# Kernel tuning notes

Measured on AMD Instinct MI355X. Metric: run time of the kernel, lower is better.

Reference implementation:

```python
import jax, jax.numpy as jnp
import numpy as np
import math

B, S, H, D = 1, 2048, 32, 128  # batch, local_seq (one ring block), num_heads, head_dim


def setup_inputs() -> dict:
    key = jax.random.key(0)
    kq, kk, kv = jax.random.split(key, 3)
    return {
        "query": jax.random.normal(kq, (B, S, H, D), dtype=jnp.float32),
        "key": jax.random.normal(kk, (B, S, H, D), dtype=jnp.float32),
        "value": jax.random.normal(kv, (B, S, H, D), dtype=jnp.float32),
    }


def reference(query, key, value):
    # RingAttention with world_size=1: a single ring step where q_block_idx == kv_block_idx,
    # i.e. standard causal attention on the local block. The online-softmax update from the
    # initial (output=0, lse=-inf) accumulator is the identity, so it is omitted.
    b, s, h, d = query.shape
    scale = 1.0 / math.sqrt(d)
    # [b, h, q, k] scores
    scores = jnp.einsum("bqhd,bkhd->bhqk", query, key) * scale
    causal = jnp.triu(jnp.ones((s, s), dtype=bool), k=1)  # True above diagonal -> masked
    scores = jnp.where(causal[None, None, :, :], -jnp.inf, scores)
    probs = jax.nn.softmax(scores, axis=-1)
    out = jnp.einsum("bhqk,bkhd->bqhd", probs, value)
    return out
```

## Files before the change

kernel.cpp:

```cpp
#include <hip/hip_runtime.h>
#include <hip/hip_bf16.h>
#include <stdint.h>

#define SEQ   2048
#define NHEAD 32
#define HDIM  128
#define RS    (NHEAD * HDIM)
#define KVBLK 64
#define NTILES (SEQ / KVBLK)
#define TILE_BYTES 16384

typedef float  f32x16 __attribute__((ext_vector_type(16)));
typedef __bf16 bf16x8 __attribute__((ext_vector_type(8)));
typedef uint32_t u32;

__device__ __forceinline__ unsigned short f2bf(float f) {
  unsigned u = __builtin_bit_cast(unsigned, f);
  u += 0x7fffu + ((u >> 16) & 1u);
  return (unsigned short)(u >> 16);
}

__device__ __forceinline__ u32 packbf(float a, float b) {
  __bf16 x = (__bf16)a, y = (__bf16)b;
  unsigned short ux = __builtin_bit_cast(unsigned short, x);
  unsigned short uy = __builtin_bit_cast(unsigned short, y);
  return (u32)ux | ((u32)uy << 16);
}

__global__ __launch_bounds__(256) void prepass_kernel(
    const float* __restrict__ K, const float* __restrict__ V,
    char* __restrict__ wsK, char* __restrict__ wsV) {
  const int tid = threadIdx.x;
  const int t   = blockIdx.x & (NTILES - 1);
  const int h   = blockIdx.x >> 5;
  const int kv0 = t * KVBLK;
  char* kd = wsK + (size_t)(h * NTILES + t) * TILE_BYTES;
  char* vd = wsV + (size_t)(h * NTILES + t) * TILE_BYTES;

  {
    const int c  = tid & 15;
    const int kr = tid >> 4;
#pragma unroll
    for (int ki = 0; ki < 4; ++ki) {
      const int kk = kr + ki * 16;
      const float* kp = K + (size_t)(kv0 + kk) * RS + h * HDIM + c * 8;
      float4 x0 = *(const float4*)kp;
      float4 x1 = *(const float4*)(kp + 4);
      uint32_t u0 = f2bf(x0.x) | ((uint32_t)f2bf(x0.y) << 16);
      uint32_t u1 = f2bf(x0.z) | ((uint32_t)f2bf(x0.w) << 16);
      uint32_t u2 = f2bf(x1.x) | ((uint32_t)f2bf(x1.y) << 16);
      uint32_t u3 = f2bf(x1.z) | ((uint32_t)f2bf(x1.w) << 16);
      const int kt = kk >> 5, n = kk & 31, ks = c >> 1, hh = c & 1;
      const uint32_t byte = (uint32_t)((kt * 8 + ks) * 1024 + (hh * 32 + n) * 16);
      *(uint4*)(kd + byte) = make_uint4(u0, u1, u2, u3);
    }
  }
  {
    const int d0  = (tid & 31) * 4;
    const int kk0 = (tid >> 5) * 8;
    float vv[8][4];
#pragma unroll
    for (int r = 0; r < 8; ++r) {
      const float* vp = V + (size_t)(kv0 + kk0 + r) * RS + h * HDIM + d0;
      float4 x = *(const float4*)vp;
      vv[r][0] = x.x; vv[r][1] = x.y; vv[r][2] = x.z; vv[r][3] = x.w;
    }
    const int s = kk0 >> 4, hh = (kk0 >> 3) & 1;
#pragma unroll
    for (int i = 0; i < 4; ++i) {
      const int d = d0 + i;
      uint32_t p0 = f2bf(vv[0][i]) | ((uint32_t)f2bf(vv[1][i]) << 16);
      uint32_t p1 = f2bf(vv[2][i]) | ((uint32_t)f2bf(vv[3][i]) << 16);
      uint32_t p2 = f2bf(vv[4][i]) | ((uint32_t)f2bf(vv[5][i]) << 16);
      uint32_t p3 = f2bf(vv[6][i]) | ((uint32_t)f2bf(vv[7][i]) << 16);
      const int nt = d >> 5;
      const uint32_t byte = (uint32_t)((s * 4 + nt) * 1024 + (hh * 32 + (d & 31)) * 16);
      *(uint4*)(vd + byte) = make_uint4(p0, p1, p2, p3);
    }
  }
}

__global__ __launch_bounds__(64, 2) void fattn_main(
    const float* __restrict__ Q, const char* __restrict__ wsK,
    const char* __restrict__ wsV, float* __restrict__ O) {
  const int lane = threadIdx.x;
  const int n    = lane & 31;
  const int hh   = lane >> 5;

  const int bid  = blockIdx.x;
  const int k    = bid >> 3;
  const int head = (bid & 7) * 4 + (k & 3);
  const int qi   = 63 - (k >> 2);
  const int ntile = (qi >> 1) + 1;
  const int qrow  = qi * 32 + n;

  const float qscale = 0.088388347648318447f * 1.4426950408889634f;

  bf16x8 bq[8];
  {
    const float* qp = Q + (size_t)qrow * RS + head * HDIM + hh * 8;
#pragma unroll
    for (int ks = 0; ks < 8; ++ks) {
      float4 v0 = *(const float4*)(qp + ks * 16);
      float4 v1 = *(const float4*)(qp + ks * 16 + 4);
      bf16x8 a;
      a[0] = (__bf16)(v0.x * qscale); a[1] = (__bf16)(v0.y * qscale);
      a[2] = (__bf16)(v0.z * qscale); a[3] = (__bf16)(v0.w * qscale);
      a[4] = (__bf16)(v1.x * qscale); a[5] = (__bf16)(v1.y * qscale);
      a[6] = (__bf16)(v1.z * qscale); a[7] = (__bf16)(v1.w * qscale);
      bq[ks] = a;
    }
  }

  f32x16 accO[4];
#pragma unroll
  for (int i = 0; i < 4; ++i) accO[i] = (f32x16)(0.f);
  float m_run  = -1e30f;
  float l_part = 0.f;

  const char* kimg = wsK + (size_t)head * NTILES * TILE_BYTES;
  const char* vimg = wsV + (size_t)head * NTILES * TILE_BYTES;

  for (int t = 0; t < ntile; ++t) {
    const char* kb = kimg + (size_t)t * TILE_BYTES + lane * 16;
    uint4 kld[16];
#pragma unroll
    for (int i = 0; i < 16; ++i) kld[i] = *(const uint4*)(kb + i * 1024);

    f32x16 sc[2];
    __builtin_amdgcn_s_setprio(1);
#pragma unroll
    for (int kt = 0; kt < 2; ++kt) {
      f32x16 acc = (f32x16)(0.f);
#pragma unroll
      for (int ks = 0; ks < 8; ++ks) {
        bf16x8 kf = __builtin_bit_cast(bf16x8, kld[kt * 8 + ks]);
        acc = __builtin_amdgcn_mfma_f32_32x32x16_bf16(kf, bq[ks], acc, 0, 0, 0);
      }
      sc[kt] = acc;
    }
    __builtin_amdgcn_s_setprio(0);

    const char* vb = vimg + (size_t)t * TILE_BYTES + lane * 16;
    uint4 vld[16];
#pragma unroll
    for (int i = 0; i < 16; ++i) vld[i] = *(const uint4*)(vb + i * 1024);

    if (t == ntile - 1) {
      const int kv0 = t * KVBLK;
#pragma unroll
      for (int kt = 0; kt < 2; ++kt)
#pragma unroll
        for (int r = 0; r < 16; ++r) {
          const int keyg = kv0 + kt * 32 + (r & 3) + 8 * (r >> 2) + 4 * hh;
          if (keyg > qrow) sc[kt][r] = -1e30f;
        }
    }

    float mx = -1e30f;
#pragma unroll
    for (int kt = 0; kt < 2; ++kt)
#pragma unroll
      for (int r = 0; r < 16; ++r) mx = fmaxf(mx, sc[kt][r]);
    mx = fmaxf(mx, __shfl_xor(mx, 32, 64));

    if (__any(mx - m_run > 11.0f)) {
      const float mn = fmaxf(m_run, mx);
      const float al = exp2f(m_run - mn);
      m_run = mn;
      l_part *= al;
#pragma unroll
      for (int r = 0; r < 16; ++r) {
        const float ar = __shfl(al, (r & 3) + 8 * (r >> 2) + 4 * hh, 64);
#pragma unroll
        for (int nt = 0; nt < 4; ++nt) accO[nt][r] *= ar;
      }
    }

    float ls = 0.f;
#pragma unroll
    for (int kt = 0; kt < 2; ++kt)
#pragma unroll
      for (int r = 0; r < 16; ++r) {
        const float p = exp2f(sc[kt][r] - m_run);
        sc[kt][r] = p;
        ls += p;
      }
    l_part += ls;

    u32 ua[2][4], ub[2][4];
#pragma unroll
    for (int kt = 0; kt < 2; ++kt)
#pragma unroll
      for (int i = 0; i < 4; ++i) {
        ua[kt][i] = packbf(sc[kt][4 * i],     sc[kt][4 * i + 1]);
        ub[kt][i] = packbf(sc[kt][4 * i + 2], sc[kt][4 * i + 3]);
      }
    u32 ra[2][2], rb[2][2];
#pragma unroll
    for (int kt = 0; kt < 2; ++kt)
#pragma unroll
      for (int q = 0; q < 2; ++q) {
        ra[kt][q] = __shfl_xor(hh ? ua[kt][2 * q] : ua[kt][2 * q + 1], 32, 64);
        rb[kt][q] = __shfl_xor(hh ? ub[kt][2 * q] : ub[kt][2 * q + 1], 32, 64);
      }

    __builtin_amdgcn_s_setprio(1);
#pragma unroll
    for (int s = 0; s < 4; ++s) {
      const int kt = s >> 1, q = s & 1;
      u32 af32[4];
      af32[0] = hh ? ra[kt][q] : ua[kt][2 * q];
      af32[1] = hh ? rb[kt][q] : ub[kt][2 * q];
      af32[2] = hh ? ua[kt][2 * q + 1] : ra[kt][q];
      af32[3] = hh ? ub[kt][2 * q + 1] : rb[kt][q];
      bf16x8 af = __builtin_bit_cast(bf16x8, *(uint4*)af32);
#pragma unroll
      for (int nt = 0; nt < 4; ++nt) {
        bf16x8 vf = __builtin_bit_cast(bf16x8, vld[s * 4 + nt]);
        accO[nt] = __builtin_amdgcn_mfma_f32_32x32x16_bf16(af, vf, accO[nt], 0, 0, 0);
      }
    }
    __builtin_amdgcn_s_setprio(0);
  }

  const float lf  = l_part + __shfl_xor(l_part, 32, 64);
  const float inv = 1.0f / lf;
  float* ob = O + (size_t)(qi * 32) * RS + head * HDIM;
#pragma unroll
  for (int r = 0; r < 16; ++r) {
    const int m = (r & 3) + 8 * (r >> 2) + 4 * hh;
    const float im = __shfl(inv, m, 64);
#pragma unroll
    for (int nt = 0; nt < 4; ++nt)
      ob[(size_t)m * RS + nt * 32 + n] = accO[nt][r] * im;
  }
}

extern "C" void kernel_launch(void* const* d_in, const int* in_sizes, int n_in,
                              void* d_out, int out_size, void* d_ws, size_t ws_size,
                              hipStream_t stream) {
  const float* q = (const float*)d_in[0];
  const float* k = (const float*)d_in[1];
  const float* v = (const float*)d_in[2];
  float* o = (float*)d_out;
  char* wsK = (char*)d_ws;
  char* wsV = wsK + (size_t)NHEAD * NTILES * TILE_BYTES;
  hipLaunchKernelGGL(prepass_kernel, dim3(NHEAD * NTILES), dim3(256), 0, stream,
                     k, v, wsK, wsV);
  hipLaunchKernelGGL(fattn_main, dim3(2048), dim3(64), 0, stream, q, wsK, wsV, o);
}
```

Measured before the change: 89.10 us.

## Prefetch next K tile and split V loads to overlap with MFMA

Loads the first K tile before the loop, then inside each iteration prefetches the next K tile after the QK^T MFMAs. V is split into two halves: the first is issued before the score MFMAs and the second after, so global load latency overlaps with compute instead of stalling each tile. The row max is also rewritten as a tree reduction to shorten the dependency chain. This raises register pressure (K prefetch plus V halves live at once), which at 2 waves per SIMD could cause spills or lower occupancy.

```diff
diff --git a/kernel.cpp b/kernel.cpp
--- a/kernel.cpp
+++ b/kernel.cpp
@@ -118,14 +118,18 @@
   float m_run  = -1e30f;
   float l_part = 0.f;
 
-  const char* kimg = wsK + (size_t)head * NTILES * TILE_BYTES;
-  const char* vimg = wsV + (size_t)head * NTILES * TILE_BYTES;
+  const char* kimg = wsK + (size_t)head * NTILES * TILE_BYTES + lane * 16;
+  const char* vimg = wsV + (size_t)head * NTILES * TILE_BYTES + lane * 16;
+
+  uint4 kld[16];
+#pragma unroll
+  for (int i = 0; i < 16; ++i) kld[i] = *(const uint4*)(kimg + i * 1024);
 
   for (int t = 0; t < ntile; ++t) {
-    const char* kb = kimg + (size_t)t * TILE_BYTES + lane * 16;
-    uint4 kld[16];
-#pragma unroll
-    for (int i = 0; i < 16; ++i) kld[i] = *(const uint4*)(kb + i * 1024);
+    const char* vb = vimg + (size_t)t * TILE_BYTES;
+    uint4 vldA[8];
+#pragma unroll
+    for (int i = 0; i < 8; ++i) vldA[i] = *(const uint4*)(vb + i * 1024);
 
     f32x16 sc[2];
     __builtin_amdgcn_s_setprio(1);
@@ -141,10 +145,15 @@
     }
     __builtin_amdgcn_s_setprio(0);
 
-    const char* vb = vimg + (size_t)t * TILE_BYTES + lane * 16;
-    uint4 vld[16];
-#pragma unroll
-    for (int i = 0; i < 16; ++i) vld[i] = *(const uint4*)(vb + i * 1024);
+    if (t + 1 < ntile) {
+      const char* kb = kimg + (size_t)(t + 1) * TILE_BYTES;
+#pragma unroll
+      for (int i = 0; i < 16; ++i) kld[i] = *(const uint4*)(kb + i * 1024);
+    }
+
+    uint4 vldB[8];
+#pragma unroll
+    for (int i = 0; i < 8; ++i) vldB[i] = *(const uint4*)(vb + (i + 8) * 1024);
 
     if (t == ntile - 1) {
       const int kv0 = t * KVBLK;
@@ -157,11 +166,14 @@
         }
     }
 
-    float mx = -1e30f;
-#pragma unroll
-    for (int kt = 0; kt < 2; ++kt)
-#pragma unroll
-      for (int r = 0; r < 16; ++r) mx = fmaxf(mx, sc[kt][r]);
+    float tm[16];
+#pragma unroll
+    for (int r = 0; r < 16; ++r) tm[r] = fmaxf(sc[0][r], sc[1][r]);
+#pragma unroll
+    for (int r = 0; r < 8; ++r) tm[r] = fmaxf(tm[r], tm[r + 8]);
+#pragma unroll
+    for (int r = 0; r < 4; ++r) tm[r] = fmaxf(tm[r], tm[r + 4]);
+    float mx = fmaxf(fmaxf(tm[0], tm[1]), fmaxf(tm[2], tm[3]));
     mx = fmaxf(mx, __shfl_xor(mx, 32, 64));
 
     if (__any(mx - m_run > 11.0f)) {
@@ -217,7 +229,8 @@
       bf16x8 af = __builtin_bit_cast(bf16x8, *(uint4*)af32);
 #pragma unroll
       for (int nt = 0; nt < 4; ++nt) {
-        bf16x8 vf = __builtin_bit_cast(bf16x8, vld[s * 4 + nt]);
+        const uint4 vchunk = (s < 2) ? vldA[s * 4 + nt] : vldB[(s - 2) * 4 + nt];
+        bf16x8 vf = __builtin_bit_cast(bf16x8, vchunk);
         accO[nt] = __builtin_amdgcn_mfma_f32_32x32x16_bf16(af, vf, accO[nt], 0, 0, 0);
       }
     }
```

New measurement: 160.4 us. +80.0%, slower.

## Split each causal query block's KV loop in two and merge partials

Applied to the files above, without the earlier changes.

Each query block's KV tiles are now processed by two workgroups, one taking even tiles and one taking odd tiles. Each writes an unnormalized fp32 partial output plus its row max and sum to workspace. A new combine kernel rescales the two partials, merges them and normalizes. The aim is more parallelism and shorter per-workgroup loops on long causal rows. The cost is about 64MB of extra partial writes and reads, one more launch, and a dependence on the workspace being large enough, with the old single-pass kernel kept as a fallback.

```diff
diff --git a/kernel.cpp b/kernel.cpp
--- a/kernel.cpp
+++ b/kernel.cpp
@@ -9,6 +9,7 @@
 #define KVBLK 64
 #define NTILES (SEQ / KVBLK)
 #define TILE_BYTES 16384
+#define IMG_BYTES ((size_t)NHEAD * NTILES * TILE_BYTES)
 
 typedef float  f32x16 __attribute__((ext_vector_type(16)));
 typedef __bf16 bf16x8 __attribute__((ext_vector_type(8)));
@@ -50,8 +51,8 @@
       uint32_t u1 = f2bf(x0.z) | ((uint32_t)f2bf(x0.w) << 16);
       uint32_t u2 = f2bf(x1.x) | ((uint32_t)f2bf(x1.y) << 16);
       uint32_t u3 = f2bf(x1.z) | ((uint32_t)f2bf(x1.w) << 16);
-      const int kt = kk >> 5, n = kk & 31, ks = c >> 1, hh = c & 1;
-      const uint32_t byte = (uint32_t)((kt * 8 + ks) * 1024 + (hh * 32 + n) * 16);
+      const int kt = kk >> 5, nn = kk & 31, ks = c >> 1, hh = c & 1;
+      const uint32_t byte = (uint32_t)((kt * 8 + ks) * 1024 + (hh * 32 + nn) * 16);
       *(uint4*)(kd + byte) = make_uint4(u0, u1, u2, u3);
     }
   }
@@ -80,149 +81,207 @@
   }
 }
 
-__global__ __launch_bounds__(64, 2) void fattn_main(
+#define FLASH_BODY(T0, STEP)                                                     \
+  for (int t = (T0); t < ntile; t += (STEP)) {                                   \
+    const char* kb = kimg + (size_t)t * TILE_BYTES;                              \
+    uint4 kld[16];                                                               \
+    _Pragma("unroll")                                                            \
+    for (int i = 0; i < 16; ++i) kld[i] = *(const uint4*)(kb + i * 1024);        \
+    f32x16 sc[2];                                                                \
+    __builtin_amdgcn_s_setprio(1);                                               \
+    _Pragma("unroll")                                                            \
+    for (int kt = 0; kt < 2; ++kt) {                                             \
+      f32x16 acc = (f32x16)(0.f);                                                \
+      _Pragma("unroll")                                                          \
+      for (int ks = 0; ks < 8; ++ks) {                                           \
+        bf16x8 kf = __builtin_bit_cast(bf16x8, kld[kt * 8 + ks]);                \
+        acc = __builtin_amdgcn_mfma_f32_32x32x16_bf16(kf, bq[ks], acc, 0, 0, 0); \
+      }                                                                          \
+      sc[kt] = acc;                                                              \
+    }                                                                            \
+    __builtin_amdgcn_s_setprio(0);                                               \
+    const char* vb = vimg + (size_t)t * TILE_BYTES;                              \
+    uint4 vld[16];                                                               \
+    _Pragma("unroll")                                                            \
+    for (int i = 0; i < 16; ++i) vld[i] = *(const uint4*)(vb + i * 1024);        \
+    if (t == ntile - 1) {                                                        \
+      const int kv0 = t * KVBLK;                                                 \
+      _Pragma("unroll")                                                          \
+      for (int kt = 0; kt < 2; ++kt)                                             \
+        _Pragma("unroll")                                                        \
+        for (int r = 0; r < 16; ++r) {                                           \
+          const int keyg = kv0 + kt * 32 + (r & 3) + 8 * (r >> 2) + 4 * hh;      \
+          if (keyg > qrow) sc[kt][r] = -1e30f;                                   \
+        }                                                                        \
+    }                                                                            \
+    float tm[16];                                                                \
+    _Pragma("unroll")                                                            \
+    for (int r = 0; r < 16; ++r) tm[r] = fmaxf(sc[0][r], sc[1][r]);              \
+    _Pragma("unroll")                                                            \
+    for (int r = 0; r < 8; ++r) tm[r] = fmaxf(tm[r], tm[r + 8]);                 \
+    _Pragma("unroll")                                                            \
+    for (int r = 0; r < 4; ++r) tm[r] = fmaxf(tm[r], tm[r + 4]);                 \
+    float mx = fmaxf(fmaxf(tm[0], tm[1]), fmaxf(tm[2], tm[3]));                  \
+    mx = fmaxf(mx, __shfl_xor(mx, 32, 64));                                      \
+    if (__any(mx - m_run > 11.0f)) {                                             \
+      const float mn = fmaxf(m_run, mx);                                         \
+      const float al = exp2f(m_run - mn);                                        \
+      m_run = mn;                                                                \
+      l_part *= al;                                                              \
+      _Pragma("unroll")                                                          \
+      for (int r = 0; r < 16; ++r) {                                             \
+        const float ar = __shfl(al, (r & 3) + 8 * (r >> 2) + 4 * hh, 64);        \
+        _Pragma("unroll")                                                        \
+        for (int nt = 0; nt < 4; ++nt) accO[nt][r] *= ar;                        \
+      }                                                                          \
+    }                                                                            \
+    float ls = 0.f;                                                              \
+    _Pragma("unroll")                                                            \
+    for (int kt = 0; kt < 2; ++kt)                                               \
+      _Pragma("unroll")                                                          \
+      for (int r = 0; r < 16; ++r) {                                             \
+        const float p = exp2f(sc[kt][r] - m_run);                                \
+        sc[kt][r] = p;                                                           \
+        ls += p;                                                                 \
+      }                                                                          \
+    l_part += ls;                                                                \
+    u32 ua[2][4], ub[2][4];                                                      \
+    _Pragma("unroll")                                                            \
+    for (int kt = 0; kt < 2; ++kt)                                               \
+      _Pragma("unroll")                                                          \
+      for (int i = 0; i < 4; ++i) {                                              \
+        ua[kt][i] = packbf(sc[kt][4 * i],     sc[kt][4 * i + 1]);                \
+        ub[kt][i] = packbf(sc[kt][4 * i + 2], sc[kt][4 * i + 3]);                \
+      }                                                                          \
+    u32 ra[2][2], rb[2][2];                                                      \
+    _Pragma("unroll")                                                            \
+    for (int kt = 0; kt < 2; ++kt)                                               \
+      _Pragma("unroll")                                                          \
+      for (int q = 0; q < 2; ++q) {                                              \
+        ra[kt][q] = __shfl_xor(hh ? ua[kt][2 * q] : ua[kt][2 * q + 1], 32, 64);  \
+        rb[kt][q] = __shfl_xor(hh ? ub[kt][2 * q] : ub[kt][2 * q + 1], 32, 64);  \
+      }                                                                          \
+    __builtin_amdgcn_s_setprio(1);                                               \
+    _Pragma("unroll")                                                            \
+    for (int s = 0; s < 4; ++s) {                                                \
+      const int kt = s >> 1, q = s & 1;                                          \
+      u32 af32[4];                                                               \
+      af32[0] = hh ? ra[kt][q] : ua[kt][2 * q];                                  \
+      af32[1] = hh ? rb[kt][q] : ub[kt][2 * q];                                  \
+      af32[2] = hh ? ua[kt][2 * q + 1] : ra[kt][q];                              \
+      af32[3] = hh ? ub[kt][2 * q + 1] : rb[kt][q];                              \
+      bf16x8 af = __builtin_bit_cast(bf16x8, *(uint4*)af32);                     \
+      _Pragma("unroll")                                                          \
+      for (int nt = 0; nt < 4; ++nt) {                                           \
+        bf16x8 vf = __builtin_bit_cast(bf16x8, vld[s * 4 + nt]);                 \
+        accO[nt] = __builtin_amdgcn_mfma_f32_32x32x16_bf16(af, vf, accO[nt], 0, 0, 0); \
+      }                                                                          \
+    }                                                                            \
+    __builtin_amdgcn_s_setprio(0);                                               \
+  }
+
+#define FLASH_PROLOG(GRID_DIV)                                                   \
+  const int lane = threadIdx.x;                                                  \
+  const int n    = lane & 31;                                                    \
+  const int hh   = lane >> 5;                                                    \
+  const float qscale = 0.088388347648318447f * 1.4426950408889634f;              \
+  bf16x8 bq[8];                                                                  \
+  {                                                                              \
+    const float* qp = Q + (size_t)qrow * RS + head * HDIM + hh * 8;              \
+    _Pragma("unroll")                                                            \
+    for (int ks = 0; ks < 8; ++ks) {                                             \
+      float4 v0 = *(const float4*)(qp + ks * 16);                                \
+      float4 v1 = *(const float4*)(qp + ks * 16 + 4);                            \
+      bf16x8 a;                                                                  \
+      a[0] = (__bf16)(v0.x * qscale); a[1] = (__bf16)(v0.y * qscale);            \
+      a[2] = (__bf16)(v0.z * qscale); a[3] = (__bf16)(v0.w * qscale);            \
+      a[4] = (__bf16)(v1.x * qscale); a[5] = (__bf16)(v1.y * qscale);            \
+      a[6] = (__bf16)(v1.z * qscale); a[7] = (__bf16)(v1.w * qscale);            \
+      bq[ks] = a;                                                                \
+    }                                                                            \
+  }                                                                              \
+  f32x16 accO[4];                                                                \
+  _Pragma("unroll")                                                              \
+  for (int i = 0; i < 4; ++i) accO[i] = (f32x16)(0.f);                           \
+  float m_run  = -1e30f;                                                         \
+  float l_part = 0.f;                                                            \
+  const char* kimg = wsK + (size_t)head * NTILES * TILE_BYTES + lane * 16;       \
+  const char* vimg = wsV + (size_t)head * NTILES * TILE_BYTES + lane * 16;
+
+__global__ __launch_bounds__(64, 2) void fattn_split(
+    const float* __restrict__ Q, const char* __restrict__ wsK,
+    const char* __restrict__ wsV, float* __restrict__ wsO,
+    float* __restrict__ wsM, float* __restrict__ wsL) {
+  const int bid  = blockIdx.x;
+  const int k    = bid >> 3;
+  const int head = (bid & 7) * 4 + (k & 3);
+  const int r_   = k >> 2;
+  const int qi   = 63 - (r_ >> 1);
+  const int half = r_ & 1;
+  const int ntile = (qi >> 1) + 1;
+  const int qrow  = qi * 32 + (threadIdx.x & 31);
+
+  FLASH_PROLOG(8)
+  FLASH_BODY(half, 2)
+
+  const float lf   = l_part + __shfl_xor(l_part, 32, 64);
+  const int   unit = (head * 64 + qi) * 2 + half;
+  float* po = wsO + (size_t)unit * 4096;
+#pragma unroll
+  for (int r = 0; r < 16; ++r) {
+    const int row = (r & 3) + 8 * (r >> 2) + 4 * hh;
+#pragma unroll
+    for (int nt = 0; nt < 4; ++nt) po[row * 128 + nt * 32 + n] = accO[nt][r];
+  }
+  if (lane < 32) { wsM[unit * 32 + lane] = m_run; wsL[unit * 32 + lane] = lf; }
+}
+
+__global__ __launch_bounds__(256) void combine_kernel(
+    const float* __restrict__ wsO, const float* __restrict__ wsM,
+    const float* __restrict__ wsL, float* __restrict__ O) {
+  const int bid  = blockIdx.x;
+  const int head = bid >> 6;
+  const int qi   = bid & 63;
+  const int t    = threadIdx.x;
+  const int row  = t >> 3;
+  const int col  = (t & 7) * 16;
+
+  const int ua = (head * 64 + qi) * 2;
+  const float m_a = wsM[ua * 32 + row],       l_a = wsL[ua * 32 + row];
+  const float m_b = wsM[(ua + 1) * 32 + row], l_b = wsL[(ua + 1) * 32 + row];
+  const float m_f = fmaxf(m_a, m_b);
+  const float aa  = exp2f(m_a - m_f);
+  const float ab  = exp2f(m_b - m_f);
+  const float inv = 1.0f / (l_a * aa + l_b * ab);
+
+  const float* pa = wsO + (size_t)ua * 4096 + row * 128 + col;
+  const float* pb = pa + 4096;
+  float* po = O + (size_t)(qi * 32 + row) * RS + head * HDIM + col;
+#pragma unroll
+  for (int i = 0; i < 4; ++i) {
+    float4 xa = *(const float4*)(pa + i * 4);
+    float4 xb = *(const float4*)(pb + i * 4);
+    float4 y;
+    y.x = (xa.x * aa + xb.x * ab) * inv;
+    y.y = (xa.y * aa + xb.y * ab) * inv;
+    y.z = (xa.z * aa + xb.z * ab) * inv;
+    y.w = (xa.w * aa + xb.w * ab) * inv;
+    *(float4*)(po + i * 4) = y;
+  }
+}
+
+__global__ __launch_bounds__(64, 2) void fattn_full(
     const float* __restrict__ Q, const char* __restrict__ wsK,
     const char* __restrict__ wsV, float* __restrict__ O) {
-  const int lane = threadIdx.x;
-  const int n    = lane & 31;
-  const int hh   = lane >> 5;
-
   const int bid  = blockIdx.x;
   const int k    = bid >> 3;
   const int head = (bid & 7) * 4 + (k & 3);
   const int qi   = 63 - (k >> 2);
   const int ntile = (qi >> 1) + 1;
-  const int qrow  = qi * 32 + n;
-
-  const float qscale = 0.088388347648318447f * 1.4426950408889634f;
-
-  bf16x8 bq[8];
-  {
-    const float* qp = Q + (size_t)qrow * RS + head * HDIM + hh * 8;
-#pragma unroll
-    for (int ks = 0; ks < 8; ++ks) {
-      float4 v0 = *(const float4*)(qp + ks * 16);
-      float4 v1 = *(const float4*)(qp + ks * 16 + 4);
-      bf16x8 a;
-      a[0] = (__bf16)(v0.x * qscale); a[1] = (__bf16)(v0.y * qscale);
-      a[2] = (__bf16)(v0.z * qscale); a[3] = (__bf16)(v0.w * qscale);
-      a[4] = (__bf16)(v1.x * qscale); a[5] = (__bf16)(v1.y * qscale);
-      a[6] = (__bf16)(v1.z * qscale); a[7] = (__bf16)(v1.w * qscale);
-      bq[ks] = a;
-    }
-  }
-
-  f32x16 accO[4];
-#pragma unroll
-  for (int i = 0; i < 4; ++i) accO[i] = (f32x16)(0.f);
-  float m_run  = -1e30f;
-  float l_part = 0.f;
-
-  const char* kimg = wsK + (size_t)head * NTILES * TILE_BYTES;
-  const char* vimg = wsV + (size_t)head * NTILES * TILE_BYTES;
-
-  for (int t = 0; t < ntile; ++t) {
-    const char* kb = kimg + (size_t)t * TILE_BYTES + lane * 16;
-    uint4 kld[16];
-#pragma unroll
-    for (int i = 0; i < 16; ++i) kld[i] = *(const uint4*)(kb + i * 1024);
-
-    f32x16 sc[2];
-    __builtin_amdgcn_s_setprio(1);
-#pragma unroll
-    for (int kt = 0; kt < 2; ++kt) {
-      f32x16 acc = (f32x16)(0.f);
-#pragma unroll
-      for (int ks = 0; ks < 8; ++ks) {
-        bf16x8 kf = __builtin_bit_cast(bf16x8, kld[kt * 8 + ks]);
-        acc = __builtin_amdgcn_mfma_f32_32x32x16_bf16(kf, bq[ks], acc, 0, 0, 0);
-      }
-      sc[kt] = acc;
-    }
-    __builtin_amdgcn_s_setprio(0);
-
-    const char* vb = vimg + (size_t)t * TILE_BYTES + lane * 16;
-    uint4 vld[16];
-#pragma unroll
-    for (int i = 0; i < 16; ++i) vld[i] = *(const uint4*)(vb + i * 1024);
-
-    if (t == ntile - 1) {
-      const int kv0 = t * KVBLK;
-#pragma unroll
-      for (int kt = 0; kt < 2; ++kt)
-#pragma unroll
-        for (int r = 0; r < 16; ++r) {
-          const int keyg = kv0 + kt * 32 + (r & 3) + 8 * (r >> 2) + 4 * hh;
-          if (keyg > qrow) sc[kt][r] = -1e30f;
-        }
-    }
-
-    float mx = -1e30f;
-#pragma unroll
-    for (int kt = 0; kt < 2; ++kt)
-#pragma unroll
-      for (int r = 0; r < 16; ++r) mx = fmaxf(mx, sc[kt][r]);
-    mx = fmaxf(mx, __shfl_xor(mx, 32, 64));
-
-    if (__any(mx - m_run > 11.0f)) {
-      const float mn = fmaxf(m_run, mx);
-      const float al = exp2f(m_run - mn);
-      m_run = mn;
-      l_part *= al;
-#pragma unroll
-      for (int r = 0; r < 16; ++r) {
-        const float ar = __shfl(al, (r & 3) + 8 * (r >> 2) + 4 * hh, 64);
-#pragma unroll
-        for (int nt = 0; nt < 4; ++nt) accO[nt][r] *= ar;
-      }
-    }
-
-    float ls = 0.f;
-#pragma unroll
-    for (int kt = 0; kt < 2; ++kt)
-#pragma unroll
-      for (int r = 0; r < 16; ++r) {
-        const float p = exp2f(sc[kt][r] - m_run);
-        sc[kt][r] = p;
-        ls += p;
-      }
-    l_part += ls;
-
-    u32 ua[2][4], ub[2][4];
-#pragma unroll
-    for (int kt = 0; kt < 2; ++kt)
-#pragma unroll
-      for (int i = 0; i < 4; ++i) {
-        ua[kt][i] = packbf(sc[kt][4 * i],     sc[kt][4 * i + 1]);
-        ub[kt][i] = packbf(sc[kt][4 * i + 2], sc[kt][4 * i + 3]);
-      }
-    u32 ra[2][2], rb[2][2];
-#pragma unroll
-    for (int kt = 0; kt < 2; ++kt)
-#pragma unroll
-      for (int q = 0; q < 2; ++q) {
-        ra[kt][q] = __shfl_xor(hh ? ua[kt][2 * q] : ua[kt][2 * q + 1], 32, 64);
-        rb[kt][q] = __shfl_xor(hh ? ub[kt][2 * q] : ub[kt][2 * q + 1], 32, 64);
-      }
-
-    __builtin_amdgcn_s_setprio(1);
-#pragma unroll
-    for (int s = 0; s < 4; ++s) {
-      const int kt = s >> 1, q = s & 1;
-      u32 af32[4];
-      af32[0] = hh ? ra[kt][q] : ua[kt][2 * q];
-      af32[1] = hh ? rb[kt][q] : ub[kt][2 * q];
-      af32[2] = hh ? ua[kt][2 * q + 1] : ra[kt][q];
-      af32[3] = hh ? ub[kt][2 * q + 1] : rb[kt][q];
-      bf16x8 af = __builtin_bit_cast(bf16x8, *(uint4*)af32);
-#pragma unroll
-      for (int nt = 0; nt < 4; ++nt) {
-        bf16x8 vf = __builtin_bit_cast(bf16x8, vld[s * 4 + nt]);
-        accO[nt] = __builtin_amdgcn_mfma_f32_32x32x16_bf16(af, vf, accO[nt], 0, 0, 0);
-      }
-    }
-    __builtin_amdgcn_s_setprio(0);
-  }
+  const int qrow  = qi * 32 + (threadIdx.x & 31);
+
+  FLASH_PROLOG(8)
+  FLASH_BODY(0, 1)
 
   const float lf  = l_part + __shfl_xor(l_part, 32, 64);
   const float inv = 1.0f / lf;
@@ -245,8 +304,24 @@
   const float* v = (const float*)d_in[2];
   float* o = (float*)d_out;
   char* wsK = (char*)d_ws;
-  char* wsV = wsK + (size_t)NHEAD * NTILES * TILE_BYTES;
+  char* wsV = wsK + IMG_BYTES;
+
+  const size_t oO = 2 * IMG_BYTES;
+  const size_t oM = oO + (size_t)4096 * 4096 * 4;
+  const size_t oL = oM + (size_t)4096 * 32 * 4;
+  const size_t need = oL + (size_t)4096 * 32 * 4;
+
   hipLaunchKernelGGL(prepass_kernel, dim3(NHEAD * NTILES), dim3(256), 0, stream,
                      k, v, wsK, wsV);
-  hipLaunchKernelGGL(fattn_main, dim3(2048), dim3(64), 0, stream, q, wsK, wsV, o);
-}
+  if (ws_size >= need) {
+    float* wsO = (float*)((char*)d_ws + oO);
+    float* wsM = (float*)((char*)d_ws + oM);
+    float* wsL = (float*)((char*)d_ws + oL);
+    hipLaunchKernelGGL(fattn_split, dim3(4096), dim3(64), 0, stream,
+                       q, wsK, wsV, wsO, wsM, wsL);
+    hipLaunchKernelGGL(combine_kernel, dim3(NHEAD * 64), dim3(256), 0, stream,
+                       wsO, wsM, wsL, o);
+  } else {
+    hipLaunchKernelGGL(fattn_full, dim3(2048), dim3(64), 0, stream, q, wsK, wsV, o);
+  }
+}
```

Result: slower. 103.8 us (+16.5%).
